# Performance work log

Hardware: AMD Instinct MI355X
Metric: run time of the kernel (lower is better)

## Reference

```python
import jax, jax.numpy as jnp
import numpy as np

B, H, W, C = 16, 256, 256, 16
HO, WO = 256, 256


def setup_inputs() -> dict:
    key = jax.random.key(0)
    k1, k2 = jax.random.split(key)
    x = jax.random.normal(k1, (B, H, W, C), dtype=jnp.float32)
    # loc network: global avg pool -> dense(C, 6); small weights, identity bias
    W_loc = jax.random.normal(k2, (C, 6), dtype=jnp.float32) * 0.01
    b_loc = jnp.asarray([1.0, 0.0, 0.0, 1.0, 0.0, 0.0], dtype=jnp.float32)
    # coords_grid = np.indices(output_grid_shape): (2, HO, WO), [0]=row idx, [1]=col idx
    coords_grid = jnp.asarray(np.indices((HO, WO), dtype=np.float32))
    return {"x": x, "W_loc": W_loc, "b_loc": b_loc, "coords_grid": coords_grid}


def _forward(x, W_loc, b_loc, coords_grid):
    # loc network: predict 6 affine params per batch element
    pooled = jnp.mean(x, axis=(1, 2))              # [B, C]
    params = pooled @ W_loc + b_loc                # [B, 6]
    A = params[:, :4].reshape(-1, 2, 2)            # [B, 2, 2]
    t = params[:, 4:]                              # [B, 2]
    # grid_transform_fn: affine map of pixel coordinates
    tc = jnp.einsum('bij,jhw->bihw', A, coords_grid) + t[:, :, None, None]  # [B,2,HO,WO]
    yc, xc = tc[:, 0], tc[:, 1]                    # [B, HO, WO] each
    # interpolation_fn: bilinear sampling with clipping (wrap=False)
    y0 = jnp.floor(yc)
    x0 = jnp.floor(xc)
    wy = yc - y0                                   # fractional weights
    wx = xc - x0
    y0i = jnp.clip(y0.astype(jnp.int32), 0, H - 1)
    y1i = jnp.clip(y0.astype(jnp.int32) + 1, 0, H - 1)
    x0i = jnp.clip(x0.astype(jnp.int32), 0, W - 1)
    x1i = jnp.clip(x0.astype(jnp.int32) + 1, 0, W - 1)
    bidx = jnp.arange(x.shape[0])[:, None, None]   # [B,1,1] batch gather index
    Ia = x[bidx, y0i, x0i]                         # [B,HO,WO,C]
    Ib = x[bidx, y0i, x1i]
    Ic = x[bidx, y1i, x0i]
    Id = x[bidx, y1i, x1i]
    wa = ((1.0 - wy) * (1.0 - wx))[..., None]
    wb = ((1.0 - wy) * wx)[..., None]
    wc = (wy * (1.0 - wx))[..., None]
    wd = (wy * wx)[..., None]
    return wa * Ia + wb * Ib + wc * Ic + wd * Id   # [B,HO,WO,C]


def reference(x, W_loc, b_loc, coords_grid):
    return _forward(x, W_loc, b_loc, coords_grid)
```

## Files before the change

### kernel.cpp

```cpp
#include <hip/hip_runtime.h>

#define BB 16
#define HH 256
#define WW 256
#define CC 16

__global__ __launch_bounds__(256) void pool_partial(const float4* __restrict__ x4,
                                                    float4* __restrict__ part) {
    __shared__ float4 smem[256];
    const int blk = blockIdx.x;
    const int tid = threadIdx.x;
    const float4* p = x4 + (size_t)blk * 4096 + tid;
    float4 acc = {0.f, 0.f, 0.f, 0.f};
#pragma unroll
    for (int k = 0; k < 16; ++k) {
        float4 v = p[k * 256];
        acc.x += v.x; acc.y += v.y; acc.z += v.z; acc.w += v.w;
    }
    smem[tid] = acc;
    __syncthreads();
    for (int s = 128; s >= 4; s >>= 1) {
        if (tid < s) {
            float4 a = smem[tid], b = smem[tid + s];
            a.x += b.x; a.y += b.y; a.z += b.z; a.w += b.w;
            smem[tid] = a;
        }
        __syncthreads();
    }
    if (tid < 4) part[blk * 4 + tid] = smem[tid];
}

__global__ __launch_bounds__(256) void compute_params(const float* __restrict__ part,
                                                      const float* __restrict__ W_loc,
                                                      const float* __restrict__ b_loc,
                                                      float* __restrict__ params) {
    __shared__ float pooled[BB][CC];
    const int tid = threadIdx.x;
    const int b = tid >> 4;
    const int c = tid & 15;
    float s = 0.f;
    for (int k = 0; k < 64; ++k)
        s += part[(((b * 64 + k) * 4) + (c >> 2)) * 4 + (c & 3)];
    pooled[b][c] = s * (1.0f / 65536.0f);
    __syncthreads();
    if (tid < BB * 6) {
        const int bb = tid / 6, j = tid % 6;
        float acc = b_loc[j];
#pragma unroll
        for (int cc = 0; cc < CC; ++cc)
            acc += pooled[bb][cc] * W_loc[cc * 6 + j];
        params[bb * 6 + j] = acc;
    }
}

__global__ __launch_bounds__(256) void sample(const float4* __restrict__ x4,
                                              const float* __restrict__ params,
                                              float4* __restrict__ out) {
    const int tid = threadIdx.x;
    const int p   = blockIdx.x * 64 + (tid >> 2);
    const int cq  = tid & 3;
    const int b   = p >> 16;
    const int hw  = p & 65535;
    const int h   = hw >> 8;
    const int w   = hw & 255;

    __shared__ float pr[6];
    if (tid < 6) pr[tid] = params[b * 6 + tid];
    __syncthreads();

    const float fh = (float)h, fw = (float)w;
    const float yc = pr[0] * fh + pr[1] * fw + pr[4];
    const float xc = pr[2] * fh + pr[3] * fw + pr[5];

    const float y0f = floorf(yc), x0f = floorf(xc);
    const float wy = yc - y0f, wx = xc - x0f;
    const int y0 = (int)y0f, x0 = (int)x0f;
    const int y0i = min(max(y0, 0), HH - 1);
    const int y1i = min(max(y0 + 1, 0), HH - 1);
    const int x0i = min(max(x0, 0), WW - 1);
    const int x1i = min(max(x0 + 1, 0), WW - 1);

    const size_t rowb = (size_t)b * (HH * WW);
    const float4* r0 = x4 + (rowb + (size_t)y0i * WW) * 4 + cq;
    const float4* r1 = x4 + (rowb + (size_t)y1i * WW) * 4 + cq;
    float4 Ia = r0[(size_t)x0i * 4];
    float4 Ib = r0[(size_t)x1i * 4];
    float4 Ic = r1[(size_t)x0i * 4];
    float4 Id = r1[(size_t)x1i * 4];

    const float wa = (1.f - wy) * (1.f - wx);
    const float wb = (1.f - wy) * wx;
    const float wc = wy * (1.f - wx);
    const float wd = wy * wx;

    float4 o;
    o.x = wa * Ia.x + wb * Ib.x + wc * Ic.x + wd * Id.x;
    o.y = wa * Ia.y + wb * Ib.y + wc * Ic.y + wd * Id.y;
    o.z = wa * Ia.z + wb * Ib.z + wc * Ic.z + wd * Id.z;
    o.w = wa * Ia.w + wb * Ib.w + wc * Ic.w + wd * Id.w;

    out[(size_t)p * 4 + cq] = o;
}

extern "C" void kernel_launch(void* const* d_in, const int* in_sizes, int n_in,
                              void* d_out, int out_size, void* d_ws, size_t ws_size,
                              hipStream_t stream) {
    const float* x     = (const float*)d_in[0];
    const float* W_loc = (const float*)d_in[1];
    const float* b_loc = (const float*)d_in[2];

    float* part   = (float*)d_ws;
    float* params = part + 16384;

    pool_partial<<<BB * 64, 256, 0, stream>>>((const float4*)x, (float4*)part);
    compute_params<<<1, 256, 0, stream>>>(part, W_loc, b_loc, params);
    sample<<<(BB * HH * WW) / 64, 256, 0, stream>>>((const float4*)x, params,
                                                    (float4*)d_out);
}
```

Before: 136.5 us.

## Fuse pooling and param computation via atomics and last-block pattern

Merges the pool-partial and compute-params kernels into one, using wave shuffles for the in-block reduction, atomic accumulation of per-batch sums, and a last-block counter that computes the affine parameters. This removes one kernel launch and the partial-sum round trip. The sampler now loads parameters directly from global memory without shared memory or a barrier, and writes output with nontemporal stores. A memset is added to zero the accumulators and counter, and float atomics make the summation order nondeterministic.

Result: slower. 170.4 us (+24.8%).

```diff
diff --git a/kernel.cpp b/kernel.cpp
--- a/kernel.cpp
+++ b/kernel.cpp
@@ -4,12 +4,23 @@
 #define HH 256
 #define WW 256
 #define CC 16
+#define NPIX (HH * WW)
+#define POOL_BLOCKS (BB * 64)
 
-__global__ __launch_bounds__(256) void pool_partial(const float4* __restrict__ x4,
-                                                    float4* __restrict__ part) {
-    __shared__ float4 smem[256];
+typedef float vfloat4 __attribute__((ext_vector_type(4)));
+
+__global__ __launch_bounds__(256) void pool_params(
+    const float4* __restrict__ x4,
+    const float* __restrict__ W_loc,
+    const float* __restrict__ b_loc,
+    float* __restrict__ sums,
+    int* __restrict__ counter,
+    float* __restrict__ params)
+{
     const int blk = blockIdx.x;
     const int tid = threadIdx.x;
+    const int b   = blk >> 6;
+
     const float4* p = x4 + (size_t)blk * 4096 + tid;
     float4 acc = {0.f, 0.f, 0.f, 0.f};
 #pragma unroll
@@ -17,60 +28,73 @@
         float4 v = p[k * 256];
         acc.x += v.x; acc.y += v.y; acc.z += v.z; acc.w += v.w;
     }
-    smem[tid] = acc;
+    for (int off = 4; off < 64; off <<= 1) {
+        acc.x += __shfl_down(acc.x, off);
+        acc.y += __shfl_down(acc.y, off);
+        acc.z += __shfl_down(acc.z, off);
+        acc.w += __shfl_down(acc.w, off);
+    }
+    __shared__ float4 wsum[4][4];
+    const int wave = tid >> 6, lane = tid & 63;
+    if (lane < 4) wsum[wave][lane] = acc;
     __syncthreads();
-    for (int s = 128; s >= 4; s >>= 1) {
-        if (tid < s) {
-            float4 a = smem[tid], b = smem[tid + s];
-            a.x += b.x; a.y += b.y; a.z += b.z; a.w += b.w;
-            smem[tid] = a;
+    if (tid < 4) {
+        float4 t0 = wsum[0][tid], t1 = wsum[1][tid];
+        float4 t2 = wsum[2][tid], t3 = wsum[3][tid];
+        float4 t;
+        t.x = t0.x + t1.x + t2.x + t3.x;
+        t.y = t0.y + t1.y + t2.y + t3.y;
+        t.z = t0.z + t1.z + t2.z + t3.z;
+        t.w = t0.w + t1.w + t2.w + t3.w;
+        atomicAdd(&sums[b * 16 + tid * 4 + 0], t.x);
+        atomicAdd(&sums[b * 16 + tid * 4 + 1], t.y);
+        atomicAdd(&sums[b * 16 + tid * 4 + 2], t.z);
+        atomicAdd(&sums[b * 16 + tid * 4 + 3], t.w);
+    }
+    __syncthreads();
+    __shared__ int isLast;
+    if (tid == 0) {
+        __threadfence();
+        int prev = atomicAdd(counter, 1);
+        isLast = (prev == POOL_BLOCKS - 1) ? 1 : 0;
+    }
+    __syncthreads();
+    if (isLast) {
+        __shared__ float pooled[BB][CC];
+        const int b2 = tid >> 4, c2 = tid & 15;
+        float v = atomicAdd(&sums[b2 * 16 + c2], 0.0f);
+        pooled[b2][c2] = v * (1.0f / 65536.0f);
+        __syncthreads();
+        if (tid < BB * 6) {
+            const int bb = tid / 6, j = tid % 6;
+            float a = b_loc[j];
+#pragma unroll
+            for (int c = 0; c < CC; ++c)
+                a += pooled[bb][c] * W_loc[c * 6 + j];
+            params[bb * 6 + j] = a;
         }
-        __syncthreads();
-    }
-    if (tid < 4) part[blk * 4 + tid] = smem[tid];
-}
-
-__global__ __launch_bounds__(256) void compute_params(const float* __restrict__ part,
-                                                      const float* __restrict__ W_loc,
-                                                      const float* __restrict__ b_loc,
-                                                      float* __restrict__ params) {
-    __shared__ float pooled[BB][CC];
-    const int tid = threadIdx.x;
-    const int b = tid >> 4;
-    const int c = tid & 15;
-    float s = 0.f;
-    for (int k = 0; k < 64; ++k)
-        s += part[(((b * 64 + k) * 4) + (c >> 2)) * 4 + (c & 3)];
-    pooled[b][c] = s * (1.0f / 65536.0f);
-    __syncthreads();
-    if (tid < BB * 6) {
-        const int bb = tid / 6, j = tid % 6;
-        float acc = b_loc[j];
-#pragma unroll
-        for (int cc = 0; cc < CC; ++cc)
-            acc += pooled[bb][cc] * W_loc[cc * 6 + j];
-        params[bb * 6 + j] = acc;
     }
 }
 
-__global__ __launch_bounds__(256) void sample(const float4* __restrict__ x4,
-                                              const float* __restrict__ params,
-                                              float4* __restrict__ out) {
+__global__ __launch_bounds__(256) void sample(
+    const float4* __restrict__ x4,
+    const float* __restrict__ params,
+    float4* __restrict__ out)
+{
     const int tid = threadIdx.x;
-    const int p   = blockIdx.x * 64 + (tid >> 2);
+    const int b   = blockIdx.x >> 10;
+    const int pix = ((blockIdx.x & 1023) << 6) + (tid >> 2);
     const int cq  = tid & 3;
-    const int b   = p >> 16;
-    const int hw  = p & 65535;
-    const int h   = hw >> 8;
-    const int w   = hw & 255;
+    const int h   = pix >> 8;
+    const int w   = pix & 255;
 
-    __shared__ float pr[6];
-    if (tid < 6) pr[tid] = params[b * 6 + tid];
-    __syncthreads();
+    const float* pr = params + b * 6;
+    const float p0 = pr[0], p1 = pr[1], p2 = pr[2];
+    const float p3 = pr[3], p4 = pr[4], p5 = pr[5];
 
     const float fh = (float)h, fw = (float)w;
-    const float yc = pr[0] * fh + pr[1] * fw + pr[4];
-    const float xc = pr[2] * fh + pr[3] * fw + pr[5];
+    const float yc = p0 * fh + p1 * fw + p4;
+    const float xc = p2 * fh + p3 * fw + p5;
 
     const float y0f = floorf(yc), x0f = floorf(xc);
     const float wy = yc - y0f, wx = xc - x0f;
@@ -80,26 +104,26 @@
     const int x0i = min(max(x0, 0), WW - 1);
     const int x1i = min(max(x0 + 1, 0), WW - 1);
 
-    const size_t rowb = (size_t)b * (HH * WW);
-    const float4* r0 = x4 + (rowb + (size_t)y0i * WW) * 4 + cq;
-    const float4* r1 = x4 + (rowb + (size_t)y1i * WW) * 4 + cq;
-    float4 Ia = r0[(size_t)x0i * 4];
-    float4 Ib = r0[(size_t)x1i * 4];
-    float4 Ic = r1[(size_t)x0i * 4];
-    float4 Id = r1[(size_t)x1i * 4];
+    const size_t base = (size_t)b * NPIX;
+    const float4* r0 = x4 + (base + (size_t)y0i * WW) * 4 + cq;
+    const float4* r1 = x4 + (base + (size_t)y1i * WW) * 4 + cq;
+    const float4 Ia = r0[(size_t)x0i * 4];
+    const float4 Ib = r0[(size_t)x1i * 4];
+    const float4 Ic = r1[(size_t)x0i * 4];
+    const float4 Id = r1[(size_t)x1i * 4];
 
     const float wa = (1.f - wy) * (1.f - wx);
     const float wb = (1.f - wy) * wx;
     const float wc = wy * (1.f - wx);
     const float wd = wy * wx;
 
-    float4 o;
+    vfloat4 o;
     o.x = wa * Ia.x + wb * Ib.x + wc * Ic.x + wd * Id.x;
     o.y = wa * Ia.y + wb * Ib.y + wc * Ic.y + wd * Id.y;
     o.z = wa * Ia.z + wb * Ib.z + wc * Ic.z + wd * Id.z;
     o.w = wa * Ia.w + wb * Ib.w + wc * Ic.w + wd * Id.w;
 
-    out[(size_t)p * 4 + cq] = o;
+    __builtin_nontemporal_store(o, (vfloat4*)&out[(base + pix) * 4 + cq]);
 }
 
 extern "C" void kernel_launch(void* const* d_in, const int* in_sizes, int n_in,
@@ -109,11 +133,16 @@
     const float* W_loc = (const float*)d_in[1];
     const float* b_loc = (const float*)d_in[2];
 
-    float* part   = (float*)d_ws;
-    float* params = part + 16384;
+    float* wsf    = (float*)d_ws;
+    float* sums   = wsf;
+    int*   counter= (int*)(wsf + 256);
+    float* params = wsf + 264;
 
-    pool_partial<<<BB * 64, 256, 0, stream>>>((const float4*)x, (float4*)part);
-    compute_params<<<1, 256, 0, stream>>>(part, W_loc, b_loc, params);
-    sample<<<(BB * HH * WW) / 64, 256, 0, stream>>>((const float4*)x, params,
-                                                    (float4*)d_out);
+    hipMemsetAsync(d_ws, 0, 257 * sizeof(float), stream);
+
+    pool_params<<<POOL_BLOCKS, 256, 0, stream>>>(
+        (const float4*)x, W_loc, b_loc, sums, counter, params);
+
+    sample<<<BB * 1024, 256, 0, stream>>>(
+        (const float4*)x, params, (float4*)d_out);
 }
```
